# Optimization experiments

Measured on AMD Instinct MI355X. Metric: run time of the kernel, lower is better.

## Reference

```python
import jax, jax.numpy as jnp
import numpy as np

N = 50000      # nodes
E = 800000     # edges (avg degree 16)
DIN = 64       # input feature dim
DOUT = 64      # output feature dim
NSLOPE = 0.2   # LeakyReLU negative slope


def setup_inputs() -> dict:
    key = jax.random.key(0)
    k1, k2, k3, k4 = jax.random.split(key, 4)
    x = jax.random.normal(k1, (N, DIN), dtype=jnp.float32)
    W = jax.random.normal(k2, (DOUT, DIN), dtype=jnp.float32) * (1.0 / np.sqrt(DIN))
    b = jnp.zeros((DOUT,), dtype=jnp.float32)
    a = jax.random.normal(k3, (DOUT,), dtype=jnp.float32) * (1.0 / np.sqrt(DOUT))
    edge_index = jax.random.randint(k4, (2, E), 0, N, dtype=jnp.int32)
    return {"x": x, "W": W, "b": b, "a": a, "edge_index": edge_index}


def reference(x, W, b, a, edge_index):
    # GATv2: e_ij = a^T LeakyReLU(W h_i + W h_j + b); softmax over incoming
    # neighbors j of node i; h_i' = sigmoid(sum_j alpha_ij * W h_j)
    Wh = x @ W.T + b                          # [N, DOUT]
    src, dst = edge_index[0], edge_index[1]   # edge j -> i
    s = Wh[dst] + Wh[src]                     # [E, DOUT] per-edge pre-activation
    e = jnp.where(s > 0, s, NSLOPE * s) @ a   # [E] attention logits
    # numerically stable segment softmax over destination nodes
    emax = jax.ops.segment_max(e, dst, num_segments=N)       # [N]
    emax = jnp.where(jnp.isfinite(emax), emax, 0.0)          # nodes with no edges
    ex = jnp.exp(e - emax[dst])                               # [E]
    denom = jax.ops.segment_sum(ex, dst, num_segments=N)      # [N]
    alpha = ex / jnp.maximum(denom[dst], 1e-9)                # [E]
    agg = jax.ops.segment_sum(alpha[:, None] * Wh[src], dst, num_segments=N)
    return jax.nn.sigmoid(agg)                # [N, DOUT]
```

## Files before the change

kernel.cpp:

```cpp
#include <hip/hip_runtime.h>
#include <hip/hip_bf16.h>
#include <math.h>

#define NN 50000
#define EE 800000
#define DD 64
#define NSLOPE 0.2f
#define NBUCK 196
#define CAP 4608
#define CHUNK 4096
#define BINB 196
#define WHB 782

__device__ __forceinline__ float leaky(float s) { return s > 0.f ? s : NSLOPE * s; }

__global__ void __launch_bounds__(256) bin_kernel(
    const int* __restrict__ ei, unsigned int* __restrict__ gbuf,
    int* __restrict__ gCursor) {
    __shared__ int cnt[256];
    __shared__ int excl[256];
    __shared__ int cur[256];
    __shared__ int base[256];
    __shared__ unsigned int pairs[CHUNK];
    int tid = threadIdx.x;
    int start = blockIdx.x * CHUNK;
    int nedge = min(CHUNK, EE - start);
    cnt[tid] = 0; cur[tid] = 0;
    __syncthreads();
    for (int j = 0; j < CHUNK / 256; ++j) {
        int i = start + tid + j * 256;
        if (i < EE) atomicAdd(&cnt[((unsigned int)ei[EE + i]) >> 8], 1);
    }
    __syncthreads();
    int v = cnt[tid];
    excl[tid] = v; __syncthreads();
    for (int o = 1; o < 256; o <<= 1) {
        int t = (tid >= o) ? excl[tid - o] : 0;
        __syncthreads();
        excl[tid] += t;
        __syncthreads();
    }
    int ex = excl[tid] - v;
    __syncthreads();
    excl[tid] = ex;
    __syncthreads();
    for (int j = 0; j < CHUNK / 256; ++j) {
        int i = start + tid + j * 256;
        if (i < EE) {
            unsigned int src = (unsigned int)ei[i];
            unsigned int dst = (unsigned int)ei[EE + i];
            int b = dst >> 8;
            int r = atomicAdd(&cur[b], 1);
            pairs[excl[b] + r] = (dst << 16) | src;
        }
    }
    if (tid < NBUCK) base[tid] = atomicAdd(&gCursor[tid], cnt[tid]);
    __syncthreads();
    for (int i = tid; i < nedge; i += 256) {
        unsigned int p = pairs[i];
        int b = p >> 24;
        gbuf[(size_t)b * CAP + base[b] + (i - excl[b])] = p;
    }
}

__global__ void __launch_bounds__(256) csr_wh_kernel(
    const unsigned int* __restrict__ gbuf, const int* __restrict__ gCursor,
    int* __restrict__ off, unsigned short* __restrict__ csr,
    const float* __restrict__ x, const float* __restrict__ W,
    const float* __restrict__ bias, float* __restrict__ Wh) {
    __shared__ __align__(16) char smem[20480];
    int tid = threadIdx.x;

    if (blockIdx.x < NBUCK) {
        int* s    = (int*)smem;
        int* hist = s + 256;
        int* excl = s + 512;
        int* cur  = s + 768;
        int k = blockIdx.x;
        int v = (tid < NBUCK) ? gCursor[tid] : 0;
        s[tid] = v; __syncthreads();
        for (int o = 1; o < 256; o <<= 1) {
            int t = (tid >= o) ? s[tid - o] : 0;
            __syncthreads();
            s[tid] += t;
            __syncthreads();
        }
        int base_k = (k == 0) ? 0 : s[k - 1];
        int cnt = s[k] - base_k;
        const unsigned int* bp = gbuf + (size_t)k * CAP;
        hist[tid] = 0; cur[tid] = 0;
        __syncthreads();
        for (int i = tid; i < cnt; i += 256)
            atomicAdd(&hist[(bp[i] >> 16) & 255], 1);
        __syncthreads();
        int hv = hist[tid];
        excl[tid] = hv; __syncthreads();
        for (int o = 1; o < 256; o <<= 1) {
            int t = (tid >= o) ? excl[tid - o] : 0;
            __syncthreads();
            excl[tid] += t;
            __syncthreads();
        }
        int hex = excl[tid] - hv;
        __syncthreads();
        excl[tid] = hex;
        __syncthreads();
        int dst = k * 256 + tid;
        if (dst < NN) off[dst] = base_k + hex;
        if (k == 0 && tid == 0) off[NN] = EE;
        for (int i = tid; i < cnt; i += 256) {
            unsigned int p = bp[i];
            int local = (p >> 16) & 255;
            int slot = base_k + excl[local] + atomicAdd(&cur[local], 1);
            csr[slot] = (unsigned short)(p & 0xffffu);
        }
        return;
    }

    int bid = blockIdx.x - NBUCK;
    float4* Wl = (float4*)smem;
    float4 (*xr)[4][16] = (float4 (*)[4][16])(smem + 16384);
    const float4* W4 = (const float4*)W;
    const float4* x4 = (const float4*)x;
    for (int i = tid; i < 1024; i += 256) {
        int c = i >> 4, k4 = i & 15;
        Wl[c * 16 + (k4 ^ (c & 15))] = W4[i];
    }
    __syncthreads();
    int wv = tid >> 6, lane = tid & 63;
    int c = lane;
    float4 wreg[16];
#pragma unroll
    for (int k4 = 0; k4 < 16; ++k4) wreg[k4] = Wl[c * 16 + (k4 ^ (c & 15))];
    float bv = bias[c];
    int l16 = lane >> 4, q = lane & 15;
    for (int rowbase = (bid * 4 + wv) * 4; rowbase < NN; rowbase += WHB * 16) {
        xr[wv][l16][q] = x4[(size_t)(rowbase + l16) * 16 + q];
        float acc0 = bv, acc1 = bv, acc2 = bv, acc3 = bv;
#pragma unroll
        for (int k4 = 0; k4 < 16; ++k4) {
            float4 w  = wreg[k4];
            float4 q0 = xr[wv][0][k4];
            float4 q1 = xr[wv][1][k4];
            float4 q2 = xr[wv][2][k4];
            float4 q3 = xr[wv][3][k4];
            acc0 += w.x * q0.x + w.y * q0.y + w.z * q0.z + w.w * q0.w;
            acc1 += w.x * q1.x + w.y * q1.y + w.z * q1.z + w.w * q1.w;
            acc2 += w.x * q2.x + w.y * q2.y + w.z * q2.z + w.w * q2.w;
            acc3 += w.x * q3.x + w.y * q3.y + w.z * q3.z + w.w * q3.w;
        }
        Wh[(size_t)(rowbase + 0) * DD + c] = acc0;
        Wh[(size_t)(rowbase + 1) * DD + c] = acc1;
        Wh[(size_t)(rowbase + 2) * DD + c] = acc2;
        Wh[(size_t)(rowbase + 3) * DD + c] = acc3;
    }
}

__global__ void __launch_bounds__(256) fused_kernel(
    const float4* __restrict__ Wh4, const float4* __restrict__ a4,
    const int* __restrict__ off, const unsigned short* __restrict__ csr,
    float4* __restrict__ out4) {
    int wave = threadIdx.x >> 6, lane = threadIdx.x & 63;
    int node = blockIdx.x * 4 + wave;
    int b = lane >> 4, f4 = lane & 15;
    float4 av  = a4[f4];
    float4 whi = Wh4[(size_t)node * 16 + f4];
    int beg = off[node], end = off[node + 1];
    float den = 0.f;
    float4 acc = make_float4(0.f, 0.f, 0.f, 0.f);
    float4 whs_n = make_float4(0.f, 0.f, 0.f, 0.f);
    if (beg < end) {
        int i0 = beg + b;
        int s0 = csr[(i0 < end) ? i0 : (end - 1)];
        whs_n = Wh4[(size_t)s0 * 16 + f4];
    }
    for (int base = beg; base < end; base += 4) {
        float4 whs = whs_n;
        int ni = base + 4 + b;
        if (ni < end) {
            int s2 = csr[ni];
            whs_n = Wh4[(size_t)s2 * 16 + f4];
        }
        float t = av.x * leaky(whi.x + whs.x) + av.y * leaky(whi.y + whs.y)
                + av.z * leaky(whi.z + whs.z) + av.w * leaky(whi.w + whs.w);
        t += __shfl_xor(t, 1, 64);
        t += __shfl_xor(t, 2, 64);
        t += __shfl_xor(t, 4, 64);
        t += __shfl_xor(t, 8, 64);
        float ex = (base + b < end) ? __expf(t) : 0.f;
        den += ex;
        acc.x += ex * whs.x; acc.y += ex * whs.y;
        acc.z += ex * whs.z; acc.w += ex * whs.w;
    }
    acc.x += __shfl_xor(acc.x, 16, 64); acc.y += __shfl_xor(acc.y, 16, 64);
    acc.z += __shfl_xor(acc.z, 16, 64); acc.w += __shfl_xor(acc.w, 16, 64);
    den   += __shfl_xor(den,   16, 64);
    acc.x += __shfl_xor(acc.x, 32, 64); acc.y += __shfl_xor(acc.y, 32, 64);
    acc.z += __shfl_xor(acc.z, 32, 64); acc.w += __shfl_xor(acc.w, 32, 64);
    den   += __shfl_xor(den,   32, 64);
    if (b == 0) {
        float id = 1.f / fmaxf(den, 1e-9f);
        float4 o;
        o.x = 1.f / (1.f + __expf(-acc.x * id));
        o.y = 1.f / (1.f + __expf(-acc.y * id));
        o.z = 1.f / (1.f + __expf(-acc.z * id));
        o.w = 1.f / (1.f + __expf(-acc.w * id));
        out4[(size_t)node * 16 + f4] = o;
    }
}

extern "C" void kernel_launch(void* const* d_in, const int* in_sizes, int n_in,
                              void* d_out, int out_size, void* d_ws, size_t ws_size,
                              hipStream_t stream) {
    const float* x = (const float*)d_in[0];
    const float* W = (const float*)d_in[1];
    const float* b = (const float*)d_in[2];
    const float* a = (const float*)d_in[3];
    const int*   ei = (const int*)d_in[4];
    float* out = (float*)d_out;

    char* ws = (char*)d_ws;
    float*          Wh      = (float*)(ws);
    int*            gCursor = (int*)(ws + 12800000);
    int*            off     = (int*)(ws + 12801024);
    unsigned int*   gbuf    = (unsigned int*)(ws + 13001216);
    unsigned short* csr     = (unsigned short*)(ws + 16613888);

    hipMemsetAsync(gCursor, 0, 1024, stream);
    bin_kernel<<<BINB, 256, 0, stream>>>(ei, gbuf, gCursor);
    csr_wh_kernel<<<NBUCK + WHB, 256, 0, stream>>>(gbuf, gCursor, off, csr,
                                                   x, W, b, Wh);
    fused_kernel<<<NN / 4, 256, 0, stream>>>((const float4*)Wh, (const float4*)a,
                                             off, csr, (float4*)out);
}
```

Baseline: 142.6 us.

## Merge pipeline into one cooperative persistent kernel with grid syncs

Result: slower. 347.0 us (+143.3%).

```diff
diff --git a/kernel.cpp b/kernel.cpp
--- a/kernel.cpp
+++ b/kernel.cpp
@@ -1,6 +1,8 @@
 #include <hip/hip_runtime.h>
-#include <hip/hip_bf16.h>
+#include <hip/hip_cooperative_groups.h>
 #include <math.h>
+
+namespace cg = cooperative_groups;
 
 #define NN 50000
 #define EE 800000
@@ -11,19 +13,19 @@
 #define CHUNK 4096
 #define BINB 196
 #define WHB 782
+#define NCU 256
 
 __device__ __forceinline__ float leaky(float s) { return s > 0.f ? s : NSLOPE * s; }
 
-__global__ void __launch_bounds__(256) bin_kernel(
-    const int* __restrict__ ei, unsigned int* __restrict__ gbuf,
-    int* __restrict__ gCursor) {
-    __shared__ int cnt[256];
-    __shared__ int excl[256];
-    __shared__ int cur[256];
-    __shared__ int base[256];
-    __shared__ unsigned int pairs[CHUNK];
-    int tid = threadIdx.x;
-    int start = blockIdx.x * CHUNK;
+__device__ __forceinline__ void bin_body(
+    int binBlk, int tid, const int* __restrict__ ei,
+    unsigned int* __restrict__ gbuf, int* __restrict__ gCursor, char* smem) {
+    int* cnt  = (int*)smem;
+    int* excl = cnt + 256;
+    int* cur  = cnt + 512;
+    int* base = cnt + 768;
+    unsigned int* pairs = (unsigned int*)(smem + 4096);
+    int start = binBlk * CHUNK;
     int nedge = min(CHUNK, EE - start);
     cnt[tid] = 0; cur[tid] = 0;
     __syncthreads();
@@ -49,75 +51,24 @@
         if (i < EE) {
             unsigned int src = (unsigned int)ei[i];
             unsigned int dst = (unsigned int)ei[EE + i];
-            int b = dst >> 8;
-            int r = atomicAdd(&cur[b], 1);
-            pairs[excl[b] + r] = (dst << 16) | src;
+            int bk = dst >> 8;
+            int r = atomicAdd(&cur[bk], 1);
+            pairs[excl[bk] + r] = (dst << 16) | src;
         }
     }
     if (tid < NBUCK) base[tid] = atomicAdd(&gCursor[tid], cnt[tid]);
     __syncthreads();
     for (int i = tid; i < nedge; i += 256) {
         unsigned int p = pairs[i];
-        int b = p >> 24;
-        gbuf[(size_t)b * CAP + base[b] + (i - excl[b])] = p;
-    }
-}
-
-__global__ void __launch_bounds__(256) csr_wh_kernel(
-    const unsigned int* __restrict__ gbuf, const int* __restrict__ gCursor,
-    int* __restrict__ off, unsigned short* __restrict__ csr,
+        int bk = p >> 24;
+        gbuf[(size_t)bk * CAP + base[bk] + (i - excl[bk])] = p;
+    }
+}
+
+__device__ __forceinline__ void wh_body(
+    int whBlk, int whStrideBlks, int tid,
     const float* __restrict__ x, const float* __restrict__ W,
-    const float* __restrict__ bias, float* __restrict__ Wh) {
-    __shared__ __align__(16) char smem[20480];
-    int tid = threadIdx.x;
-
-    if (blockIdx.x < NBUCK) {
-        int* s    = (int*)smem;
-        int* hist = s + 256;
-        int* excl = s + 512;
-        int* cur  = s + 768;
-        int k = blockIdx.x;
-        int v = (tid < NBUCK) ? gCursor[tid] : 0;
-        s[tid] = v; __syncthreads();
-        for (int o = 1; o < 256; o <<= 1) {
-            int t = (tid >= o) ? s[tid - o] : 0;
-            __syncthreads();
-            s[tid] += t;
-            __syncthreads();
-        }
-        int base_k = (k == 0) ? 0 : s[k - 1];
-        int cnt = s[k] - base_k;
-        const unsigned int* bp = gbuf + (size_t)k * CAP;
-        hist[tid] = 0; cur[tid] = 0;
-        __syncthreads();
-        for (int i = tid; i < cnt; i += 256)
-            atomicAdd(&hist[(bp[i] >> 16) & 255], 1);
-        __syncthreads();
-        int hv = hist[tid];
-        excl[tid] = hv; __syncthreads();
-        for (int o = 1; o < 256; o <<= 1) {
-            int t = (tid >= o) ? excl[tid - o] : 0;
-            __syncthreads();
-            excl[tid] += t;
-            __syncthreads();
-        }
-        int hex = excl[tid] - hv;
-        __syncthreads();
-        excl[tid] = hex;
-        __syncthreads();
-        int dst = k * 256 + tid;
-        if (dst < NN) off[dst] = base_k + hex;
-        if (k == 0 && tid == 0) off[NN] = EE;
-        for (int i = tid; i < cnt; i += 256) {
-            unsigned int p = bp[i];
-            int local = (p >> 16) & 255;
-            int slot = base_k + excl[local] + atomicAdd(&cur[local], 1);
-            csr[slot] = (unsigned short)(p & 0xffffu);
-        }
-        return;
-    }
-
-    int bid = blockIdx.x - NBUCK;
+    const float* __restrict__ bias, float* __restrict__ Wh, char* smem) {
     float4* Wl = (float4*)smem;
     float4 (*xr)[4][16] = (float4 (*)[4][16])(smem + 16384);
     const float4* W4 = (const float4*)W;
@@ -134,7 +85,8 @@
     for (int k4 = 0; k4 < 16; ++k4) wreg[k4] = Wl[c * 16 + (k4 ^ (c & 15))];
     float bv = bias[c];
     int l16 = lane >> 4, q = lane & 15;
-    for (int rowbase = (bid * 4 + wv) * 4; rowbase < NN; rowbase += WHB * 16) {
+    for (int rowbase = (whBlk * 4 + wv) * 4; rowbase < NN;
+         rowbase += whStrideBlks * 16) {
         xr[wv][l16][q] = x4[(size_t)(rowbase + l16) * 16 + q];
         float acc0 = bv, acc1 = bv, acc2 = bv, acc3 = bv;
 #pragma unroll
@@ -156,27 +108,73 @@
     }
 }
 
-__global__ void __launch_bounds__(256) fused_kernel(
-    const float4* __restrict__ Wh4, const float4* __restrict__ a4,
+__device__ __forceinline__ void csr_body(
+    int k, int tid, const unsigned int* __restrict__ gbuf,
+    const int* __restrict__ gCursor, int* __restrict__ off,
+    unsigned short* __restrict__ csr, char* smem) {
+    int* s    = (int*)smem;
+    int* hist = s + 256;
+    int* excl = s + 512;
+    int* cur  = s + 768;
+    int v = (tid < NBUCK) ? gCursor[tid] : 0;
+    s[tid] = v; __syncthreads();
+    for (int o = 1; o < 256; o <<= 1) {
+        int t = (tid >= o) ? s[tid - o] : 0;
+        __syncthreads();
+        s[tid] += t;
+        __syncthreads();
+    }
+    int base_k = (k == 0) ? 0 : s[k - 1];
+    int cnt = s[k] - base_k;
+    const unsigned int* bp = gbuf + (size_t)k * CAP;
+    hist[tid] = 0; cur[tid] = 0;
+    __syncthreads();
+    for (int i = tid; i < cnt; i += 256)
+        atomicAdd(&hist[(bp[i] >> 16) & 255], 1);
+    __syncthreads();
+    int hv = hist[tid];
+    excl[tid] = hv; __syncthreads();
+    for (int o = 1; o < 256; o <<= 1) {
+        int t = (tid >= o) ? excl[tid - o] : 0;
+        __syncthreads();
+        excl[tid] += t;
+        __syncthreads();
+    }
+    int hex = excl[tid] - hv;
+    __syncthreads();
+    excl[tid] = hex;
+    __syncthreads();
+    int dst = k * 256 + tid;
+    if (dst < NN) off[dst] = base_k + hex;
+    if (k == 0 && tid == 0) off[NN] = EE;
+    for (int i = tid; i < cnt; i += 256) {
+        unsigned int p = bp[i];
+        int local = (p >> 16) & 255;
+        int slot = base_k + excl[local] + atomicAdd(&cur[local], 1);
+        csr[slot] = (unsigned short)(p & 0xffffu);
+    }
+}
+
+__device__ __forceinline__ void fused_group(
+    int g, int tid, const float4* __restrict__ Wh4, float4 av,
     const int* __restrict__ off, const unsigned short* __restrict__ csr,
     float4* __restrict__ out4) {
-    int wave = threadIdx.x >> 6, lane = threadIdx.x & 63;
-    int node = blockIdx.x * 4 + wave;
-    int b = lane >> 4, f4 = lane & 15;
-    float4 av  = a4[f4];
+    int wave = tid >> 6, lane = tid & 63;
+    int eb = lane >> 4, f4 = lane & 15;
+    int node = g * 4 + wave;
     float4 whi = Wh4[(size_t)node * 16 + f4];
     int beg = off[node], end = off[node + 1];
     float den = 0.f;
     float4 acc = make_float4(0.f, 0.f, 0.f, 0.f);
     float4 whs_n = make_float4(0.f, 0.f, 0.f, 0.f);
     if (beg < end) {
-        int i0 = beg + b;
+        int i0 = beg + eb;
         int s0 = csr[(i0 < end) ? i0 : (end - 1)];
         whs_n = Wh4[(size_t)s0 * 16 + f4];
     }
     for (int base = beg; base < end; base += 4) {
         float4 whs = whs_n;
-        int ni = base + 4 + b;
+        int ni = base + 4 + eb;
         if (ni < end) {
             int s2 = csr[ni];
             whs_n = Wh4[(size_t)s2 * 16 + f4];
@@ -187,7 +185,7 @@
         t += __shfl_xor(t, 2, 64);
         t += __shfl_xor(t, 4, 64);
         t += __shfl_xor(t, 8, 64);
-        float ex = (base + b < end) ? __expf(t) : 0.f;
+        float ex = (base + eb < end) ? __expf(t) : 0.f;
         den += ex;
         acc.x += ex * whs.x; acc.y += ex * whs.y;
         acc.z += ex * whs.z; acc.w += ex * whs.w;
@@ -198,7 +196,7 @@
     acc.x += __shfl_xor(acc.x, 32, 64); acc.y += __shfl_xor(acc.y, 32, 64);
     acc.z += __shfl_xor(acc.z, 32, 64); acc.w += __shfl_xor(acc.w, 32, 64);
     den   += __shfl_xor(den,   32, 64);
-    if (b == 0) {
+    if (eb == 0) {
         float id = 1.f / fmaxf(den, 1e-9f);
         float4 o;
         o.x = 1.f / (1.f + __expf(-acc.x * id));
@@ -209,12 +207,70 @@
     }
 }
 
+__global__ void __launch_bounds__(256, 4) mega_kernel(
+    const int* __restrict__ ei, unsigned int* __restrict__ gbuf,
+    int* __restrict__ gCursor, int* __restrict__ off,
+    unsigned short* __restrict__ csr,
+    const float* __restrict__ x, const float* __restrict__ W,
+    const float* __restrict__ bias, const float* __restrict__ a,
+    float* __restrict__ Wh, float* __restrict__ out) {
+    cg::grid_group grid = cg::this_grid();
+    __shared__ __align__(16) char smem[20480];
+    int tid = threadIdx.x;
+    int G = (int)gridDim.x;
+
+    if (blockIdx.x < BINB)
+        bin_body(blockIdx.x, tid, ei, gbuf, gCursor, smem);
+    else
+        wh_body(blockIdx.x - BINB, G - BINB, tid, x, W, bias, Wh, smem);
+
+    grid.sync();
+
+    if (blockIdx.x < NBUCK)
+        csr_body(blockIdx.x, tid, gbuf, gCursor, off, csr, smem);
+
+    grid.sync();
+
+    const float4* Wh4  = (const float4*)Wh;
+    float4*       out4 = (float4*)out;
+    float4 av = ((const float4*)a)[tid & 15];
+    for (int g = blockIdx.x; g < NN / 4; g += G)
+        fused_group(g, tid, Wh4, av, off, csr, out4);
+}
+
+__global__ void __launch_bounds__(256) bin_kernel(
+    const int* __restrict__ ei, unsigned int* __restrict__ gbuf,
+    int* __restrict__ gCursor) {
+    __shared__ __align__(16) char smem[20480];
+    bin_body(blockIdx.x, threadIdx.x, ei, gbuf, gCursor, smem);
+}
+
+__global__ void __launch_bounds__(256) csr_wh_kernel(
+    const unsigned int* __restrict__ gbuf, const int* __restrict__ gCursor,
+    int* __restrict__ off, unsigned short* __restrict__ csr,
+    const float* __restrict__ x, const float* __restrict__ W,
+    const float* __restrict__ bias, float* __restrict__ Wh) {
+    __shared__ __align__(16) char smem[20480];
+    if (blockIdx.x < NBUCK)
+        csr_body(blockIdx.x, threadIdx.x, gbuf, gCursor, off, csr, smem);
+    else
+        wh_body(blockIdx.x - NBUCK, WHB, threadIdx.x, x, W, bias, Wh, smem);
+}
+
+__global__ void __launch_bounds__(256) fused_kernel(
+    const float4* __restrict__ Wh4, const float4* __restrict__ a4,
+    const int* __restrict__ off, const unsigned short* __restrict__ csr,
+    float4* __restrict__ out4) {
+    float4 av = a4[threadIdx.x & 15];
+    fused_group(blockIdx.x, threadIdx.x, Wh4, av, off, csr, out4);
+}
+
 extern "C" void kernel_launch(void* const* d_in, const int* in_sizes, int n_in,
                               void* d_out, int out_size, void* d_ws, size_t ws_size,
                               hipStream_t stream) {
     const float* x = (const float*)d_in[0];
     const float* W = (const float*)d_in[1];
-    const float* b = (const float*)d_in[2];
+    const float* bias = (const float*)d_in[2];
     const float* a = (const float*)d_in[3];
     const int*   ei = (const int*)d_in[4];
     float* out = (float*)d_out;
@@ -227,9 +283,26 @@
     unsigned short* csr     = (unsigned short*)(ws + 16613888);
 
     hipMemsetAsync(gCursor, 0, 1024, stream);
-    bin_kernel<<<BINB, 256, 0, stream>>>(ei, gbuf, gCursor);
-    csr_wh_kernel<<<NBUCK + WHB, 256, 0, stream>>>(gbuf, gCursor, off, csr,
-                                                   x, W, b, Wh);
-    fused_kernel<<<NN / 4, 256, 0, stream>>>((const float4*)Wh, (const float4*)a,
-                                             off, csr, (float4*)out);
-}
+
+    int nb = 0;
+    hipError_t oerr = hipOccupancyMaxActiveBlocksPerMultiprocessor(
+        &nb, mega_kernel, 256, 0);
+    int G = (oerr == hipSuccess) ? nb * NCU : 0;
+    if (G > 1024) G = 1024;
+    hipError_t lerr = hipErrorUnknown;
+    if (G >= BINB + 64) {
+        void* args[] = {(void*)&ei, (void*)&gbuf, (void*)&gCursor, (void*)&off,
+                        (void*)&csr, (void*)&x, (void*)&W, (void*)&bias,
+                        (void*)&a, (void*)&Wh, (void*)&out};
+        lerr = hipLaunchCooperativeKernel((const void*)mega_kernel, dim3(G),
+                                          dim3(256), args, 0, stream);
+    }
+    if (lerr != hipSuccess) {
+        bin_kernel<<<BINB, 256, 0, stream>>>(ei, gbuf, gCursor);
+        csr_wh_kernel<<<NBUCK + WHB, 256, 0, stream>>>(gbuf, gCursor, off, csr,
+                                                       x, W, bias, Wh);
+        fused_kernel<<<NN / 4, 256, 0, stream>>>((const float4*)Wh,
+                                                 (const float4*)a, off, csr,
+                                                 (float4*)out);
+    }
+}
```
